# Kernel optimization log

Hardware: AMD Instinct MI355X
Metric: run time of the kernel (lower is better)

## Reference

```python
import jax, jax.numpy as jnp
import numpy as np

N_NODES = 100000
N_EDGES = 1600000
D_IN = 264
D_HID = 64
NEG_SLOPE = 0.2


def _glorot(key, shape):
    fan_in, fan_out = shape[0], shape[-1]
    lim = jnp.sqrt(6.0 / (fan_in + fan_out))
    return jax.random.uniform(key, shape, jnp.float32, -lim, lim)


def setup_inputs() -> dict:
    key = jax.random.key(0)
    ks = jax.random.split(key, 24)
    x = jax.random.normal(ks[0], (N_NODES, D_IN), jnp.float32)
    src = jax.random.randint(ks[1], (N_EDGES,), 0, N_NODES, jnp.int32)
    off = jax.random.randint(ks[2], (N_EDGES,), 1, N_NODES, jnp.int32)
    dst = (src + off) % N_NODES  # guaranteed no self loops
    edge_index = jnp.stack([src, dst], axis=0)
    edge_attr = jax.random.normal(ks[3], (N_EDGES, 1), jnp.float32)
    p = {
        'l1_Wl': _glorot(ks[4], (D_IN, D_HID)), 'l1_bl': jnp.zeros((D_HID,), jnp.float32),
        'l1_Wr': _glorot(ks[5], (D_IN, D_HID)), 'l1_br': jnp.zeros((D_HID,), jnp.float32),
        'l1_We': _glorot(ks[6], (1, D_HID)),
        'l1_att': _glorot(ks[7], (1, 1, D_HID)), 'l1_bias': jnp.zeros((D_HID,), jnp.float32),
        'l2_Wl': _glorot(ks[8], (D_HID, D_HID)), 'l2_bl': jnp.zeros((D_HID,), jnp.float32),
        'l2_Wr': _glorot(ks[9], (D_HID, D_HID)), 'l2_br': jnp.zeros((D_HID,), jnp.float32),
        'l2_We': _glorot(ks[10], (1, D_HID)),
        'l2_att': _glorot(ks[11], (1, 1, D_HID)), 'l2_bias': jnp.zeros((D_HID,), jnp.float32),
        'W3': _glorot(ks[12], (D_HID, D_HID)), 'b3': jnp.zeros((D_HID,), jnp.float32),
        'W4': _glorot(ks[13], (D_HID, 1)), 'b4': jnp.zeros((1,), jnp.float32),
    }
    return dict(x=x, edge_index=edge_index, edge_attr=edge_attr, **p)


def _gatv2_layer(x, src, dst, ea, Wl, bl, Wr, br, We, att, bias):
    # heads=1, concat=True, aggr='max' (passed via **kwargs to MessagePassing)
    n = x.shape[0]
    xl = (x @ Wl + bl).reshape(n, 1, D_HID)  # source-side transform
    xr = (x @ Wr + br).reshape(n, 1, D_HID)  # target-side transform
    e = (ea @ We).reshape(-1, 1, D_HID)      # lin_edge, no bias
    m = jax.nn.leaky_relu(xr[dst] + xl[src] + e, NEG_SLOPE)  # (Etot,1,64)
    logits = jnp.sum(m * att, axis=-1)       # (Etot,1)
    # segment softmax over destination nodes
    mx = jax.ops.segment_max(logits, dst, num_segments=n)
    ex = jnp.exp(logits - mx[dst])
    den = jax.ops.segment_sum(ex, dst, num_segments=n)
    alpha = ex / den[dst]                    # (Etot,1)
    msg = xl[src] * alpha[:, :, None]        # (Etot,1,64)
    out = jax.ops.segment_max(msg, dst, num_segments=n)  # aggr='max'
    return out.reshape(n, D_HID) + bias


def _gcn_forward(x, src, dst, edge_attr,
                 l1_Wl, l1_bl, l1_Wr, l1_br, l1_We, l1_att, l1_bias,
                 l2_Wl, l2_bl, l2_Wr, l2_br, l2_We, l2_att, l2_bias,
                 W3, b3, W4, b4):
    n = x.shape[0]
    # add_self_loops with fill_value='mean' (edges contain no self loops)
    loop = jnp.arange(n, dtype=src.dtype)
    src2 = jnp.concatenate([src, loop])
    dst2 = jnp.concatenate([dst, loop])
    mean_ea = jnp.mean(edge_attr, axis=0, keepdims=True)  # (1,1)
    ea2 = jnp.concatenate([edge_attr, jnp.broadcast_to(mean_ea, (n, 1))], axis=0)
    h = _gatv2_layer(x, src2, dst2, ea2, l1_Wl, l1_bl, l1_Wr, l1_br, l1_We, l1_att, l1_bias)
    h = jax.nn.relu(h)  # dropout inactive in eval
    h = _gatv2_layer(h, src2, dst2, ea2, l2_Wl, l2_bl, l2_Wr, l2_br, l2_We, l2_att, l2_bias)
    h = jax.nn.relu(h)
    h = jax.nn.relu(h @ W3 + b3)
    h = h @ W4 + b4
    return jnp.squeeze(h, axis=-1)  # (N,)


def reference(x, edge_index, edge_attr,
              l1_Wl, l1_bl, l1_Wr, l1_br, l1_We, l1_att, l1_bias,
              l2_Wl, l2_bl, l2_Wr, l2_br, l2_We, l2_att, l2_bias,
              W3, b3, W4, b4):
    src, dst = edge_index[0], edge_index[1]
    return _gcn_forward(x, src, dst, edge_attr,
                        l1_Wl, l1_bl, l1_Wr, l1_br, l1_We, l1_att, l1_bias,
                        l2_Wl, l2_bl, l2_Wr, l2_br, l2_We, l2_att, l2_bias,
                        W3, b3, W4, b4)
```

## Files before the change

### kernel.cpp

```cpp
#include <hip/hip_runtime.h>
#include <math.h>
#include <float.h>

#define NN 100000
#define NE 1600000
#define ETOT 1700000
#define DIN 264
#define DH 64
#define SLOPE 0.2f
#define NB 98

typedef __attribute__((ext_vector_type(8))) short s8v;
typedef __attribute__((ext_vector_type(4))) float f4v;

__device__ __forceinline__ unsigned short f2bf(float x) {
  unsigned u = __float_as_uint(x);
  u += 0x7FFFu + ((u >> 16) & 1u);
  return (unsigned short)(u >> 16);
}
__device__ __forceinline__ float bf2f(unsigned short h) {
  return __uint_as_float(((unsigned)h) << 16);
}

__global__ void k_mean(const float* __restrict__ ea, float* __restrict__ sum) {
  float acc = 0.f;
  for (int i = blockIdx.x * blockDim.x + threadIdx.x; i < NE; i += gridDim.x * blockDim.x)
    acc += ea[i];
  #pragma unroll
  for (int off = 32; off > 0; off >>= 1) acc += __shfl_xor(acc, off);
  __shared__ float s[4];
  int lane = threadIdx.x & 63, w = threadIdx.x >> 6;
  if (lane == 0) s[w] = acc;
  __syncthreads();
  if (threadIdx.x == 0) atomicAdd(sum, s[0] + s[1] + s[2] + s[3]);
}

__global__ void k_hist(const int* __restrict__ ei, unsigned* __restrict__ deg) {
  int e = blockIdx.x * blockDim.x + threadIdx.x;
  if (e >= ETOT) return;
  int d = (e < NE) ? ei[NE + e] : e - NE;
  atomicAdd(&deg[d], 1u);
}

__global__ __launch_bounds__(256)
void k_bsum(const unsigned* __restrict__ deg, unsigned* __restrict__ bsum) {
  int i0 = blockIdx.x * 1024 + threadIdx.x * 4;
  unsigned s = 0;
  if (i0 + 3 < NN) {
    uint4 v = *(const uint4*)&deg[i0];
    s = v.x + v.y + v.z + v.w;
  }
  #pragma unroll
  for (int off = 32; off > 0; off >>= 1) s += __shfl_xor(s, off);
  __shared__ unsigned ws[4];
  int lane = threadIdx.x & 63, w = threadIdx.x >> 6;
  if (lane == 0) ws[w] = s;
  __syncthreads();
  if (threadIdx.x == 0) bsum[blockIdx.x] = ws[0] + ws[1] + ws[2] + ws[3];
}

__global__ __launch_bounds__(128)
void k_sscan(unsigned* __restrict__ bsum, unsigned* __restrict__ rowptr) {
  __shared__ unsigned ls[128];
  int t = threadIdx.x;
  unsigned v = (t < NB) ? bsum[t] : 0u;
  ls[t] = v;
  __syncthreads();
  for (int off = 1; off < 128; off <<= 1) {
    unsigned u = (t >= off) ? ls[t - off] : 0u;
    __syncthreads();
    ls[t] += u;
    __syncthreads();
  }
  if (t < NB) bsum[t] = ls[t] - v;
  if (t == 127) rowptr[NN] = ls[127];
}

__global__ __launch_bounds__(256)
void k_scan2(const unsigned* __restrict__ deg, const unsigned* __restrict__ bsum,
             unsigned* __restrict__ rowptr, unsigned* __restrict__ wptr) {
  __shared__ unsigned ls[256];
  int i0 = blockIdx.x * 1024 + threadIdx.x * 4;
  unsigned d0 = 0, d1 = 0, d2 = 0, d3 = 0;
  if (i0 + 3 < NN) {
    uint4 v = *(const uint4*)&deg[i0];
    d0 = v.x; d1 = v.y; d2 = v.z; d3 = v.w;
  }
  unsigned ts = d0 + d1 + d2 + d3;
  ls[threadIdx.x] = ts;
  __syncthreads();
  for (int off = 1; off < 256; off <<= 1) {
    unsigned u = (threadIdx.x >= (unsigned)off) ? ls[threadIdx.x - off] : 0u;
    __syncthreads();
    ls[threadIdx.x] += u;
    __syncthreads();
  }
  unsigned base = bsum[blockIdx.x] + ls[threadIdx.x] - ts;
  if (i0 + 3 < NN) {
    uint4 r;
    r.x = base;
    r.y = base + d0;
    r.z = r.y + d1;
    r.w = r.z + d2;
    *(uint4*)&rowptr[i0] = r;
    *(uint4*)&wptr[i0] = r;
  }
}

__global__ void k_scatter(const int* __restrict__ ei, const float* __restrict__ ea,
                          const float* __restrict__ sump, unsigned* __restrict__ wptr,
                          int2* __restrict__ csr) {
  int e = blockIdx.x * blockDim.x + threadIdx.x;
  if (e >= ETOT) return;
  int s, d;
  float a;
  if (e < NE) {
    s = ei[e];
    d = ei[NE + e];
    a = ea[e];
  } else {
    s = d = e - NE;
    a = sump[0] * (1.0f / NE);
  }
  unsigned pos = atomicAdd(&wptr[d], 1u);
  csr[pos] = make_int2(s, __float_as_int(a));
}

template <int K>
__global__ __launch_bounds__(256)
void k_wprep(const float* __restrict__ Wl, const float* __restrict__ Wr,
             unsigned short* __restrict__ wfh, unsigned short* __restrict__ wfl) {
  constexpr int KC = (K + 31) / 32;
  int t = blockIdx.x * blockDim.x + threadIdx.x;
  if (t >= 8 * KC * 64) return;
  int lane = t & 63;
  int kc = (t >> 6) % KC;
  int ntg = t / (64 * KC);
  const float* src = (ntg < 4) ? Wl : Wr;
  int n = (ntg & 3) * 16 + (lane & 15);
  int k0 = kc * 32 + (lane >> 4) * 8;
  #pragma unroll
  for (int i = 0; i < 8; i++) {
    int k = k0 + i;
    float v = (k < K) ? src[k * DH + n] : 0.f;
    unsigned short hh = f2bf(v);
    wfh[t * 8 + i] = hh;
    wfl[t * 8 + i] = f2bf(v - bf2f(hh));
  }
}

template <int K>
__global__ __launch_bounds__(256) __attribute__((amdgpu_waves_per_eu(2)))
void k_mm(const float* __restrict__ X,
          const unsigned short* __restrict__ wfh, const unsigned short* __restrict__ wfl,
          const float* __restrict__ bl, const float* __restrict__ br,
          float* __restrict__ xl, float* __restrict__ xr) {
  constexpr int KC = (K + 31) / 32;
  constexpr int KP = KC * 32;
  constexpr int SP = KP + 8;
  __shared__ unsigned short lsh[64 * SP];
  __shared__ unsigned short lsl[64 * SP];
  const int r0 = blockIdx.x * 64;
  const int tid = threadIdx.x;
  if constexpr (KP > K) {
    constexpr int PADW = (KP - K) / 2;
    for (int t = tid; t < 64 * PADW; t += 256) {
      int row = t / PADW, c = t - row * PADW;
      *(unsigned*)&lsh[row * SP + K + 2 * c] = 0u;
      *(unsigned*)&lsl[row * SP + K + 2 * c] = 0u;
    }
  }
  {
    constexpr int HK = K / 2;
    for (int p = tid; p < 64 * HK; p += 256) {
      int row = p / HK, kp = p - row * HK;
      int grow = r0 + row;
      float a = 0.f, b = 0.f;
      if (grow < NN) {
        float2 v = *(const float2*)&X[(size_t)grow * K + 2 * kp];
        a = v.x; b = v.y;
      }
      unsigned short ha = f2bf(a), hb = f2bf(b);
      unsigned short la = f2bf(a - bf2f(ha)), lb = f2bf(b - bf2f(hb));
      *(unsigned*)&lsh[row * SP + 2 * kp] = (unsigned)ha | ((unsigned)hb << 16);
      *(unsigned*)&lsl[row * SP + 2 * kp] = (unsigned)la | ((unsigned)lb << 16);
    }
  }
  __syncthreads();
  const int lane = tid & 63, w = tid >> 6;
  const int kq = lane >> 4;
  const int ar = lane & 15;
  f4v acc[4][2];
  #pragma unroll
  for (int mt = 0; mt < 4; mt++)
    #pragma unroll
    for (int j = 0; j < 2; j++)
      acc[mt][j] = (f4v){0.f, 0.f, 0.f, 0.f};
  for (int kc = 0; kc < KC; kc++) {
    const int kb = kc * 32 + kq * 8;
    s8v ah[4], al[4];
    #pragma unroll
    for (int mt = 0; mt < 4; mt++) {
      ah[mt] = *(const s8v*)&lsh[(mt * 16 + ar) * SP + kb];
      al[mt] = *(const s8v*)&lsl[(mt * 16 + ar) * SP + kb];
    }
    #pragma unroll
    for (int j = 0; j < 2; j++) {
      const int bidx = (((w * 2 + j) * KC + kc) * 64 + lane) * 8;
      s8v bh = *(const s8v*)&wfh[bidx];
      s8v bv = *(const s8v*)&wfl[bidx];
      #pragma unroll
      for (int mt = 0; mt < 4; mt++) {
        acc[mt][j] = __builtin_amdgcn_mfma_f32_16x16x32_bf16(ah[mt], bh, acc[mt][j], 0, 0, 0);
        acc[mt][j] = __builtin_amdgcn_mfma_f32_16x16x32_bf16(ah[mt], bv, acc[mt][j], 0, 0, 0);
        acc[mt][j] = __builtin_amdgcn_mfma_f32_16x16x32_bf16(al[mt], bh, acc[mt][j], 0, 0, 0);
      }
    }
  }
  const int mat = w >> 1;
  const float* bias = mat ? br : bl;
  float* outp = mat ? xr : xl;
  #pragma unroll
  for (int j = 0; j < 2; j++) {
    int col = ((w & 1) * 2 + j) * 16 + ar;
    float bv = bias[col];
    #pragma unroll
    for (int mt = 0; mt < 4; mt++) {
      #pragma unroll
      for (int r = 0; r < 4; r++) {
        int grow = r0 + mt * 16 + kq * 4 + r;
        if (grow < NN) outp[(size_t)grow * DH + col] = acc[mt][j][r] + bv;
      }
    }
  }
}

template <bool HEAD>
__global__ void k_attn(const unsigned* __restrict__ rowptr, const int2* __restrict__ csr,
                       const float* __restrict__ xl, const float* __restrict__ xr,
                       const float* __restrict__ We, const float* __restrict__ att,
                       const float* __restrict__ bias, float* __restrict__ h,
                       const float* __restrict__ W3, const float* __restrict__ b3,
                       const float* __restrict__ W4, const float* __restrict__ b4,
                       float* __restrict__ out) {
  int n = (blockIdx.x * blockDim.x + threadIdx.x) >> 4;
  int l = threadIdx.x & 15;
  int g0 = threadIdx.x & 48;
  if (n >= NN) return;
  int l4 = l * 4;
  float4 xr4 = *(const float4*)&xr[n * DH + l4];
  float4 we4 = *(const float4*)&We[l4];
  float4 at4 = *(const float4*)&att[l4];
  int beg = rowptr[n], end = rowptr[n + 1];
  float M, D;
  float4 V;
  {
    int2 c0 = csr[beg];
    float a = __int_as_float(c0.y);
    float4 sl = *(const float4*)&xl[c0.x * DH + l4];
    float v, p = 0.f;
    v = xr4.x + sl.x + a * we4.x; v = v > 0.f ? v : SLOPE * v; p += v * at4.x;
    v = xr4.y + sl.y + a * we4.y; v = v > 0.f ? v : SLOPE * v; p += v * at4.y;
    v = xr4.z + sl.z + a * we4.z; v = v > 0.f ? v : SLOPE * v; p += v * at4.z;
    v = xr4.w + sl.w + a * we4.w; v = v > 0.f ? v : SLOPE * v; p += v * at4.w;
    p += __shfl_xor(p, 1);
    p += __shfl_xor(p, 2);
    p += __shfl_xor(p, 4);
    p += __shfl_xor(p, 8);
    M = p; D = 1.f; V = sl;
  }
  for (int e0 = beg + 1; e0 < end; e0 += 16) {
    int2 cl = csr[min(e0 + l, end - 1)];
    int cnt = min(16, end - e0);
    for (int i = 0; i < cnt; i += 4) {
      int mm = min(4, cnt - i);
      float4 sl[4];
      float av[4];
      #pragma unroll
      for (int j = 0; j < 4; j++) {
        if (j < mm) {
          int s = __shfl(cl.x, g0 + i + j);
          av[j] = __int_as_float(__shfl(cl.y, g0 + i + j));
          sl[j] = *(const float4*)&xl[s * DH + l4];
        }
      }
      #pragma unroll
      for (int j = 0; j < 4; j++) {
        if (j < mm) {
          float a = av[j];
          float v, p = 0.f;
          v = xr4.x + sl[j].x + a * we4.x; v = v > 0.f ? v : SLOPE * v; p += v * at4.x;
          v = xr4.y + sl[j].y + a * we4.y; v = v > 0.f ? v : SLOPE * v; p += v * at4.y;
          v = xr4.z + sl[j].z + a * we4.z; v = v > 0.f ? v : SLOPE * v; p += v * at4.z;
          v = xr4.w + sl[j].w + a * we4.w; v = v > 0.f ? v : SLOPE * v; p += v * at4.w;
          p += __shfl_xor(p, 1);
          p += __shfl_xor(p, 2);
          p += __shfl_xor(p, 4);
          p += __shfl_xor(p, 8);
          float Mn = fmaxf(M, p);
          float sO = __expf(M - Mn), sN = __expf(p - Mn);
          D = D * sO + sN;
          V.x = fmaxf(V.x * sO, sl[j].x * sN);
          V.y = fmaxf(V.y * sO, sl[j].y * sN);
          V.z = fmaxf(V.z * sO, sl[j].z * sN);
          V.w = fmaxf(V.w * sO, sl[j].w * sN);
          M = Mn;
        }
      }
    }
  }
  float inv = 1.0f / D;
  float4 b = *(const float4*)&bias[l4];
  float4 o;
  o.x = fmaxf(V.x * inv + b.x, 0.f);
  o.y = fmaxf(V.y * inv + b.y, 0.f);
  o.z = fmaxf(V.z * inv + b.z, 0.f);
  o.w = fmaxf(V.w * inv + b.w, 0.f);
  if (!HEAD) {
    *(float4*)&h[n * DH + l4] = o;
  } else {
    float4 acc = {0.f, 0.f, 0.f, 0.f};
    #pragma unroll
    for (int kk = 0; kk < 16; kk++) {
      float4 hk;
      hk.x = __shfl(o.x, g0 + kk);
      hk.y = __shfl(o.y, g0 + kk);
      hk.z = __shfl(o.z, g0 + kk);
      hk.w = __shfl(o.w, g0 + kk);
      float4 w0 = *(const float4*)&W3[(kk * 4 + 0) * DH + l4];
      acc.x = fmaf(hk.x, w0.x, acc.x);
      acc.y = fmaf(hk.x, w0.y, acc.y);
      acc.z = fmaf(hk.x, w0.z, acc.z);
      acc.w = fmaf(hk.x, w0.w, acc.w);
      float4 w1 = *(const float4*)&W3[(kk * 4 + 1) * DH + l4];
      acc.x = fmaf(hk.y, w1.x, acc.x);
      acc.y = fmaf(hk.y, w1.y, acc.y);
      acc.z = fmaf(hk.y, w1.z, acc.z);
      acc.w = fmaf(hk.y, w1.w, acc.w);
      float4 w2 = *(const float4*)&W3[(kk * 4 + 2) * DH + l4];
      acc.x = fmaf(hk.z, w2.x, acc.x);
      acc.y = fmaf(hk.z, w2.y, acc.y);
      acc.z = fmaf(hk.z, w2.z, acc.z);
      acc.w = fmaf(hk.z, w2.w, acc.w);
      float4 w3 = *(const float4*)&W3[(kk * 4 + 3) * DH + l4];
      acc.x = fmaf(hk.w, w3.x, acc.x);
      acc.y = fmaf(hk.w, w3.y, acc.y);
      acc.z = fmaf(hk.w, w3.z, acc.z);
      acc.w = fmaf(hk.w, w3.w, acc.w);
    }
    float4 b3v = *(const float4*)&b3[l4];
    float4 w4v = *(const float4*)&W4[l4];
    float t, p = 0.f;
    t = acc.x + b3v.x; t = t > 0.f ? t : 0.f; p += t * w4v.x;
    t = acc.y + b3v.y; t = t > 0.f ? t : 0.f; p += t * w4v.y;
    t = acc.z + b3v.z; t = t > 0.f ? t : 0.f; p += t * w4v.z;
    t = acc.w + b3v.w; t = t > 0.f ? t : 0.f; p += t * w4v.w;
    p += __shfl_xor(p, 1);
    p += __shfl_xor(p, 2);
    p += __shfl_xor(p, 4);
    p += __shfl_xor(p, 8);
    if (l == 0) out[n] = p + b4[0];
  }
}

extern "C" void kernel_launch(void* const* d_in, const int* in_sizes, int n_in,
                              void* d_out, int out_size, void* d_ws, size_t ws_size,
                              hipStream_t stream) {
  const float* x      = (const float*)d_in[0];
  const int*   ei     = (const int*)d_in[1];
  const float* ea     = (const float*)d_in[2];
  const float* l1_Wl  = (const float*)d_in[3];
  const float* l1_bl  = (const float*)d_in[4];
  const float* l1_Wr  = (const float*)d_in[5];
  const float* l1_br  = (const float*)d_in[6];
  const float* l1_We  = (const float*)d_in[7];
  const float* l1_att = (const float*)d_in[8];
  const float* l1_bias= (const float*)d_in[9];
  const float* l2_Wl  = (const float*)d_in[10];
  const float* l2_bl  = (const float*)d_in[11];
  const float* l2_Wr  = (const float*)d_in[12];
  const float* l2_br  = (const float*)d_in[13];
  const float* l2_We  = (const float*)d_in[14];
  const float* l2_att = (const float*)d_in[15];
  const float* l2_bias= (const float*)d_in[16];
  const float* W3     = (const float*)d_in[17];
  const float* b3     = (const float*)d_in[18];
  const float* W4     = (const float*)d_in[19];
  const float* b4     = (const float*)d_in[20];
  float* out = (float*)d_out;

  float*    ws     = (float*)d_ws;
  float*    sum    = ws;
  float*    xl     = ws + 256;
  float*    xr     = xl + NN * DH;
  float*    h      = xr + NN * DH;
  int2*     csr    = (int2*)(h + NN * DH);
  unsigned* rowptr = (unsigned*)(csr + ETOT);
  unsigned* wptr   = rowptr + NN + 4;
  unsigned* deg    = wptr + NN;
  unsigned* bsum   = deg + NN;
  unsigned short* wf1h = (unsigned short*)(bsum + 128);
  unsigned short* wf1l = wf1h + 36864;
  unsigned short* wf2h = wf1l + 36864;
  unsigned short* wf2l = wf2h + 8192;

  const int B = 256;
  const int mm_blocks   = (NN + 63) / 64;
  const int edge_blocks = (ETOT + B - 1) / B;
  const int attn_blocks = (NN * 16) / B;

  hipMemsetAsync(sum, 0, 256 * sizeof(float), stream);
  hipMemsetAsync(deg, 0, NN * sizeof(unsigned), stream);
  k_wprep<DIN><<<(8 * 9 * 64 + B - 1) / B, B, 0, stream>>>(l1_Wl, l1_Wr, wf1h, wf1l);
  k_wprep<DH><<<(8 * 2 * 64 + B - 1) / B, B, 0, stream>>>(l2_Wl, l2_Wr, wf2h, wf2l);
  k_mean<<<256, B, 0, stream>>>(ea, sum);
  k_hist<<<edge_blocks, B, 0, stream>>>(ei, deg);
  k_bsum<<<NB, B, 0, stream>>>(deg, bsum);
  k_sscan<<<1, 128, 0, stream>>>(bsum, rowptr);
  k_scan2<<<NB, B, 0, stream>>>(deg, bsum, rowptr, wptr);
  k_scatter<<<edge_blocks, B, 0, stream>>>(ei, ea, sum, wptr, csr);

  k_mm<DIN><<<mm_blocks, B, 0, stream>>>(x, wf1h, wf1l, l1_bl, l1_br, xl, xr);
  k_attn<false><<<attn_blocks, B, 0, stream>>>(rowptr, csr, xl, xr, l1_We, l1_att,
                                               l1_bias, h, W3, b3, W4, b4, out);

  k_mm<DH><<<mm_blocks, B, 0, stream>>>(h, wf2h, wf2l, l2_bl, l2_br, xl, xr);
  k_attn<true><<<attn_blocks, B, 0, stream>>>(rowptr, csr, xl, xr, l2_We, l2_att,
                                              l2_bias, h, W3, b3, W4, b4, out);
}
```

Measured before the change: 710.5 us.

## Use 512-thread blocks in k_mm with one column tile per wave and preloaded weights

The projection GEMM kernel now runs 8 waves per block instead of 4, and each wave owns a single 16-column tile instead of two. All of a wave's weight fragments (hi and lo bf16 parts) are loaded into registers before the X tile is staged to shared memory, so those global loads overlap the staging phase. The k loop is fully unrolled, and A fragments are read from LDS per MFMA group rather than buffered. The goals are more waves in flight and better latency hiding. The cost is more register pressure from holding KC weight fragments (9 chunks for the 264-wide input), and each A fragment is now read from LDS by 8 waves instead of 4.

Result: faster. 661.9 us (-6.8%).

```diff
diff --git a/kernel.cpp b/kernel.cpp
--- a/kernel.cpp
+++ b/kernel.cpp
@@ -150,7 +150,7 @@
 }
 
 template <int K>
-__global__ __launch_bounds__(256) __attribute__((amdgpu_waves_per_eu(2)))
+__global__ __launch_bounds__(512) __attribute__((amdgpu_waves_per_eu(4)))
 void k_mm(const float* __restrict__ X,
           const unsigned short* __restrict__ wfh, const unsigned short* __restrict__ wfl,
           const float* __restrict__ bl, const float* __restrict__ br,
@@ -162,9 +162,21 @@
   __shared__ unsigned short lsl[64 * SP];
   const int r0 = blockIdx.x * 64;
   const int tid = threadIdx.x;
+  const int lane = tid & 63, w = tid >> 6;
+  const int kq = lane >> 4;
+  const int ar = lane & 15;
+
+  s8v bh[KC], bv[KC];
+  #pragma unroll
+  for (int kc = 0; kc < KC; kc++) {
+    const int bidx = ((w * KC + kc) * 64 + lane) * 8;
+    bh[kc] = *(const s8v*)&wfh[bidx];
+    bv[kc] = *(const s8v*)&wfl[bidx];
+  }
+
   if constexpr (KP > K) {
     constexpr int PADW = (KP - K) / 2;
-    for (int t = tid; t < 64 * PADW; t += 256) {
+    for (int t = tid; t < 64 * PADW; t += 512) {
       int row = t / PADW, c = t - row * PADW;
       *(unsigned*)&lsh[row * SP + K + 2 * c] = 0u;
       *(unsigned*)&lsl[row * SP + K + 2 * c] = 0u;
@@ -172,7 +184,7 @@
   }
   {
     constexpr int HK = K / 2;
-    for (int p = tid; p < 64 * HK; p += 256) {
+    for (int p = tid; p < 64 * HK; p += 512) {
       int row = p / HK, kp = p - row * HK;
       int grow = r0 + row;
       float a = 0.f, b = 0.f;
@@ -187,50 +199,33 @@
     }
   }
   __syncthreads();
-  const int lane = tid & 63, w = tid >> 6;
-  const int kq = lane >> 4;
-  const int ar = lane & 15;
-  f4v acc[4][2];
-  #pragma unroll
-  for (int mt = 0; mt < 4; mt++)
-    #pragma unroll
-    for (int j = 0; j < 2; j++)
-      acc[mt][j] = (f4v){0.f, 0.f, 0.f, 0.f};
+
+  f4v acc[4];
+  #pragma unroll
+  for (int mt = 0; mt < 4; mt++) acc[mt] = (f4v){0.f, 0.f, 0.f, 0.f};
+  #pragma unroll
   for (int kc = 0; kc < KC; kc++) {
     const int kb = kc * 32 + kq * 8;
-    s8v ah[4], al[4];
     #pragma unroll
     for (int mt = 0; mt < 4; mt++) {
-      ah[mt] = *(const s8v*)&lsh[(mt * 16 + ar) * SP + kb];
-      al[mt] = *(const s8v*)&lsl[(mt * 16 + ar) * SP + kb];
-    }
+      s8v ah = *(const s8v*)&lsh[(mt * 16 + ar) * SP + kb];
+      s8v al = *(const s8v*)&lsl[(mt * 16 + ar) * SP + kb];
+      acc[mt] = __builtin_amdgcn_mfma_f32_16x16x32_bf16(ah, bh[kc], acc[mt], 0, 0, 0);
+      acc[mt] = __builtin_amdgcn_mfma_f32_16x16x32_bf16(ah, bv[kc], acc[mt], 0, 0, 0);
+      acc[mt] = __builtin_amdgcn_mfma_f32_16x16x32_bf16(al, bh[kc], acc[mt], 0, 0, 0);
+    }
+  }
+
+  const float* bias = (w < 4) ? bl : br;
+  float* outp = (w < 4) ? xl : xr;
+  const int col = (w & 3) * 16 + ar;
+  const float bvv = bias[col];
+  #pragma unroll
+  for (int mt = 0; mt < 4; mt++) {
     #pragma unroll
-    for (int j = 0; j < 2; j++) {
-      const int bidx = (((w * 2 + j) * KC + kc) * 64 + lane) * 8;
-      s8v bh = *(const s8v*)&wfh[bidx];
-      s8v bv = *(const s8v*)&wfl[bidx];
-      #pragma unroll
-      for (int mt = 0; mt < 4; mt++) {
-        acc[mt][j] = __builtin_amdgcn_mfma_f32_16x16x32_bf16(ah[mt], bh, acc[mt][j], 0, 0, 0);
-        acc[mt][j] = __builtin_amdgcn_mfma_f32_16x16x32_bf16(ah[mt], bv, acc[mt][j], 0, 0, 0);
-        acc[mt][j] = __builtin_amdgcn_mfma_f32_16x16x32_bf16(al[mt], bh, acc[mt][j], 0, 0, 0);
-      }
-    }
-  }
-  const int mat = w >> 1;
-  const float* bias = mat ? br : bl;
-  float* outp = mat ? xr : xl;
-  #pragma unroll
-  for (int j = 0; j < 2; j++) {
-    int col = ((w & 1) * 2 + j) * 16 + ar;
-    float bv = bias[col];
-    #pragma unroll
-    for (int mt = 0; mt < 4; mt++) {
-      #pragma unroll
-      for (int r = 0; r < 4; r++) {
-        int grow = r0 + mt * 16 + kq * 4 + r;
-        if (grow < NN) outp[(size_t)grow * DH + col] = acc[mt][j][r] + bv;
-      }
+    for (int r = 0; r < 4; r++) {
+      int grow = r0 + mt * 16 + kq * 4 + r;
+      if (grow < NN) outp[(size_t)grow * DH + col] = acc[mt][r] + bvv;
     }
   }
 }
@@ -420,11 +415,11 @@
   k_scan2<<<NB, B, 0, stream>>>(deg, bsum, rowptr, wptr);
   k_scatter<<<edge_blocks, B, 0, stream>>>(ei, ea, sum, wptr, csr);
 
-  k_mm<DIN><<<mm_blocks, B, 0, stream>>>(x, wf1h, wf1l, l1_bl, l1_br, xl, xr);
+  k_mm<DIN><<<mm_blocks, 512, 0, stream>>>(x, wf1h, wf1l, l1_bl, l1_br, xl, xr);
   k_attn<false><<<attn_blocks, B, 0, stream>>>(rowptr, csr, xl, xr, l1_We, l1_att,
                                                l1_bias, h, W3, b3, W4, b4, out);
 
-  k_mm<DH><<<mm_blocks, B, 0, stream>>>(h, wf2h, wf2l, l2_bl, l2_br, xl, xr);
+  k_mm<DH><<<mm_blocks, 512, 0, stream>>>(h, wf2h, wf2l, l2_bl, l2_br, xl, xr);
   k_attn<true><<<attn_blocks, B, 0, stream>>>(rowptr, csr, xl, xr, l2_We, l2_att,
                                               l2_bias, h, W3, b3, W4, b4, out);
 }
```
